# Performance work log

Measured on AMD Instinct MI355X. Metric: run time of the kernel, lower is better.

The kernel has to match this reference:

```python
import jax, jax.numpy as jnp
import numpy as np

LEAK = 0.01  # torch LeakyReLU default negative_slope
HALF_LOG_2PI = 0.5 * float(np.log(2.0 * np.pi))


def setup_inputs() -> dict:
    key = jax.random.key(0)
    ks = jax.random.split(key, 5)
    N, D = 8192, 512
    H = 2 * D
    x = jax.random.normal(ks[0], (N, D), dtype=jnp.float32)
    # small init so exp(logvar/2) stays well-behaved (mimics trained-net scale)
    W1 = jax.random.normal(ks[1], (H, H), dtype=jnp.float32) * 0.02
    b1 = jnp.zeros((H,), dtype=jnp.float32)
    W2 = jax.random.normal(ks[2], (H, H), dtype=jnp.float32) * 0.02
    b2 = jnp.zeros((H,), dtype=jnp.float32)
    eps = jax.random.normal(ks[3], (N, D), dtype=jnp.float32)
    return {"x": x, "W1": W1, "b1": b1, "W2": W2, "b2": b2, "eps": eps, "n": 4}


def reference(x, W1, b1, W2, b2, eps, n):
    N, D = x.shape
    # pairwise squared distances via the expansion identity (avoids [N,N,D] diff)
    sq = jnp.sum(x * x, axis=1)                       # [N]
    d = sq[:, None] + sq[None, :] - 2.0 * (x @ x.T)   # [N, N]
    # argsort(d)[:, :n] == indices of the n smallest distances per row
    _, subsets = jax.lax.top_k(-d, n)                 # [N, n]
    z = x[subsets]                                    # [N, n, D] gather
    mu_pool = jnp.mean(z, axis=1)                     # [N, D]
    mx_pool = jnp.max(z, axis=1)                      # [N, D]
    h = jnp.concatenate((mu_pool, mx_pool), axis=1)   # [N, 2D]
    # decoder: Linear -> LeakyReLU -> Linear (torch Linear: h @ W.T + b)
    h = h @ W1.T + b1
    h = jnp.where(h >= 0, h, LEAK * h)
    h = h @ W2.T + b2
    mu = h[:, :D]
    sigma = jnp.exp(h[:, D:] * 0.5)
    x_out = x + mu + sigma * eps                      # rsample
    entropy = jnp.mean(0.5 + HALF_LOG_2PI + jnp.log(sigma))
    rows = jnp.repeat(jnp.arange(N), n)
    sub_idx = (rows, subsets.reshape(-1))
    return (x_out, entropy, sub_idx)
```

## Files before the change

kernel.cpp:

```cpp
#include <hip/hip_runtime.h>
#include <math.h>

#define N_ROWS 8192
#define DIM 512
#define HID 1024
#define NSPLIT 16
#define SPLITC 512
#define NCT 4

typedef _Float16 f16x8 __attribute__((ext_vector_type(8)));
typedef _Float16 f16x4 __attribute__((ext_vector_type(4)));
typedef float f32x4 __attribute__((ext_vector_type(4)));

__device__ __forceinline__ bool dj_less(float d1, int j1, float d2, int j2) {
  return (d1 < d2) || (d1 == d2 && j1 < j2);
}
__device__ __forceinline__ unsigned umin32(unsigned a, unsigned b) { return a < b ? a : b; }
__device__ __forceinline__ unsigned umax32(unsigned a, unsigned b) { return a > b ? a : b; }

__device__ __forceinline__ void gload_lds16(const void* g, void* s) {
  __builtin_amdgcn_global_load_lds((const __attribute__((address_space(1))) void*)g,
                                   (__attribute__((address_space(3))) void*)s, 16, 0, 0);
}

#define S_SWZ(r) ((((r) & 3) ^ (((r) >> 2) & 3)))

#define INS4(K, xin)                                   \
  {                                                    \
    unsigned xx = (xin), t;                            \
    t = umin32(K[0], xx); xx = umax32(K[0], xx); K[0] = t; \
    t = umin32(K[1], xx); xx = umax32(K[1], xx); K[1] = t; \
    t = umin32(K[2], xx); xx = umax32(K[2], xx); K[2] = t; \
    K[3] = umin32(K[3], xx);                           \
  }

__global__ __launch_bounds__(256) void convert_kernel(const float* __restrict__ x,
                                                      const float* __restrict__ W1,
                                                      const float* __restrict__ W2,
                                                      _Float16* __restrict__ xh,
                                                      _Float16* __restrict__ W1f,
                                                      _Float16* __restrict__ W2f,
                                                      float* __restrict__ sq) {
  int bid = blockIdx.x;
  int tid = threadIdx.x;
  if (bid < 4096) {
    int g = bid * 256 + tid;
    float4 v = reinterpret_cast<const float4*>(x)[g];
    f16x4 hv = {(_Float16)v.x, (_Float16)v.y, (_Float16)v.z, (_Float16)v.w};
    reinterpret_cast<f16x4*>(xh)[g] = hv;
    float s = v.x * v.x + v.y * v.y + v.z * v.z + v.w * v.w;
    for (int off = 32; off > 0; off >>= 1) s += __shfl_down(s, off);
    __shared__ float red[4];
    if ((tid & 63) == 0) red[tid >> 6] = s;
    __syncthreads();
    if (tid == 0) sq[bid * 2] = red[0] + red[1];
    if (tid == 128) sq[bid * 2 + 1] = red[2] + red[3];
  } else {
    const float* src = (bid < 5120) ? W1 : W2;
    _Float16* dst = (bid < 5120) ? W1f : W2f;
    int g = ((bid < 5120) ? (bid - 4096) : (bid - 5120)) * 256 + tid;
    float4 v = reinterpret_cast<const float4*>(src)[g];
    f16x4 h = {(_Float16)v.x, (_Float16)v.y, (_Float16)v.z, (_Float16)v.w};
    reinterpret_cast<f16x4*>(dst)[g] = h;
  }
}

__global__ __launch_bounds__(256, 4) void dist_cand_mfma(const _Float16* __restrict__ xh,
                                                         const float* __restrict__ sq,
                                                         unsigned int* __restrict__ cand) {
  __shared__ __align__(16) char smem[34816];
  unsigned* DkA = (unsigned*)(smem + 16384);
  unsigned* DkB = (unsigned*)(smem + 25600);
  const int tid = threadIdx.x;
  const int lane = tid & 63;
  const int w = tid >> 6;
  const int wm = w >> 1, wn = w & 1;
  const int row0 = blockIdx.x * 128;
  const int js = blockIdx.y;

  int a_off[4], b_off[4];
#pragma unroll
  for (int m = 0; m < 4; ++m) {
    int r = wm * 64 + m * 16 + (lane & 15);
    a_off[m] = r * 64 + (((lane >> 4) ^ S_SWZ(r)) * 16);
  }
#pragma unroll
  for (int n = 0; n < 4; ++n) {
    int r = wn * 64 + n * 16 + (lane & 15);
    b_off[n] = r * 64 + (((lane >> 4) ^ S_SWZ(r)) * 16);
  }

  int goff[2], wb[2];
#pragma unroll
  for (int h = 0; h < 2; ++h) {
    int i = h * 256 + tid;
    int r = i >> 2, cs = i & 3;
    int c = cs ^ S_SWZ(r);
    goff[h] = r * 512 + c * 8;
    wb[h] = h * 4096 + w * 1024;
  }

  const int sr = tid >> 2;
  const int sc = tid & 3;
  const int slot = wn * 16 + (lane & 15);

  unsigned keys[2][4];
#pragma unroll
  for (int p = 0; p < 2; ++p)
#pragma unroll
    for (int q = 0; q < 4; ++q) keys[p][q] = 0xFFFFFFFFu;

  const _Float16* arow = xh + (size_t)row0 * DIM;

  f32x4 acc[4][4];

  auto stage = [&](int b, const _Float16* br, int kt) {
#pragma unroll
    for (int h = 0; h < 2; ++h) {
      int go = goff[h] + kt * 32;
      gload_lds16(arow + go, smem + b * 16384 + wb[h]);
      gload_lds16(br + go, smem + b * 16384 + 8192 + wb[h]);
    }
  };
  auto compute = [&](int b) {
    f16x8 bf[4];
#pragma unroll
    for (int n = 0; n < 4; ++n) bf[n] = *(const f16x8*)(smem + b * 16384 + 8192 + b_off[n]);
#pragma unroll
    for (int m = 0; m < 4; ++m) {
      f16x8 af = *(const f16x8*)(smem + b * 16384 + a_off[m]);
#pragma unroll
      for (int n = 0; n < 4; ++n)
        acc[m][n] = __builtin_amdgcn_mfma_f32_16x16x32_f16(af, bf[n], acc[m][n], 0, 0, 0);
    }
  };

  stage(0, xh + (size_t)(js * SPLITC) * DIM, 0);
  __syncthreads();

#pragma unroll 1
  for (int ct = 0; ct < NCT; ++ct) {
    const int c0 = js * SPLITC + ct * 128;
    const _Float16* brow = xh + (size_t)c0 * DIM;
#pragma unroll
    for (int m = 0; m < 4; ++m)
#pragma unroll
      for (int n = 0; n < 4; ++n) acc[m][n] = (f32x4)0.0f;

#pragma unroll 1
    for (int k = 0; k < 8; ++k) {
      stage(1, brow, 2 * k + 1);
      compute(0);
      __syncthreads();
      if (k < 7) stage(0, brow, 2 * k + 2);
      compute(1);
      __syncthreads();
    }

    stage(0, xh + (size_t)(js * SPLITC + ((ct + 1) & (NCT - 1)) * 128) * DIM, 0);

    float sqjb[4];
#pragma unroll
    for (int n = 0; n < 4; ++n) sqjb[n] = sq[c0 + wn * 64 + n * 16 + (lane & 15)] + 1024.0f;

#pragma unroll
    for (int p = 0; p < 2; ++p) {
      if (wm == p) {
#pragma unroll
        for (int m = 0; m < 4; ++m)
#pragma unroll
          for (int j = 0; j < 4; ++j) {
            int rl = m * 16 + ((lane >> 4) << 2) + j;
            unsigned u[4];
#pragma unroll
            for (int n = 0; n < 4; ++n) {
              float v = fmaf(-2.0f, acc[m][n][j], sqjb[n]);
              u[n] = (__float_as_uint(v) & 0xFFFFE000u) |
                     (unsigned)(c0 + wn * 64 + n * 16 + (lane & 15));
            }
            unsigned lo01 = umin32(u[0], u[1]), hi01 = umax32(u[0], u[1]);
            unsigned lo23 = umin32(u[2], u[3]), hi23 = umax32(u[2], u[3]);
            DkA[rl * 36 + slot] = umin32(lo01, lo23);
            DkB[rl * 36 + slot] = umin32(umax32(lo01, lo23), umin32(hi01, hi23));
          }
      }
      __syncthreads();
      {
        const uint4* pa = (const uint4*)&DkA[sr * 36 + sc * 8];
        const uint4* pb = (const uint4*)&DkB[sr * 36 + sc * 8];
        uint4 a0 = pa[0], a1 = pa[1], b0 = pb[0], b1 = pb[1];
        INS4(keys[p], a0.x); INS4(keys[p], a0.y); INS4(keys[p], a0.z); INS4(keys[p], a0.w);
        INS4(keys[p], a1.x); INS4(keys[p], a1.y); INS4(keys[p], a1.z); INS4(keys[p], a1.w);
        INS4(keys[p], b0.x); INS4(keys[p], b0.y); INS4(keys[p], b0.z); INS4(keys[p], b0.w);
        INS4(keys[p], b1.x); INS4(keys[p], b1.y); INS4(keys[p], b1.z); INS4(keys[p], b1.w);
      }
      __syncthreads();
    }
  }

#pragma unroll
  for (int p = 0; p < 2; ++p) {
    int row = row0 + p * 64 + sr;
    uint4 o;
    o.x = keys[p][0]; o.y = keys[p][1]; o.z = keys[p][2]; o.w = keys[p][3];
    *reinterpret_cast<uint4*>(&cand[(size_t)row * 256 + js * 16 + sc * 4]) = o;
  }
}

__global__ __launch_bounds__(64) void rescore_pool_kernel(const float* __restrict__ x,
                                                          const float* __restrict__ sq,
                                                          const unsigned int* __restrict__ cand,
                                                          float* __restrict__ orows,
                                                          float* __restrict__ osubs,
                                                          _Float16* __restrict__ h0) {
  const int row = blockIdx.x;
  const int lane = threadIdx.x;
  uint4 q = *reinterpret_cast<const uint4*>(&cand[(size_t)row * 256 + lane * 4]);
  unsigned cur = q.x, c1 = q.y, c2 = q.z, c3 = q.w;
  unsigned myj = 0;
#pragma unroll 1
  for (int r = 0; r < 16; ++r) {
    unsigned mn = cur;
#pragma unroll
    for (int off = 32; off > 0; off >>= 1)
      mn = umin32(mn, (unsigned)__shfl_xor((int)mn, off));
    if (cur == mn) { cur = c1; c1 = c2; c2 = c3; c3 = 0xFFFFFFFFu; }
    if (lane == r) myj = mn & 0x1FFFu;
  }

  const float4* xi = reinterpret_cast<const float4*>(x + (size_t)row * DIM);
  float4 xa = xi[lane];
  float4 xb = xi[lane + 64];
  float sqi = sq[row];

  float dme = 0.0f;
  int jme = 0;
#pragma unroll 1
  for (int c = 0; c < 16; ++c) {
    int j = __shfl((int)myj, c);
    const float4* xj = reinterpret_cast<const float4*>(x + (size_t)j * DIM);
    float4 ya = xj[lane];
    float4 yb = xj[lane + 64];
    float dot = xa.x * ya.x + xa.y * ya.y + xa.z * ya.z + xa.w * ya.w +
                xb.x * yb.x + xb.y * yb.y + xb.z * yb.z + xb.w * yb.w;
#pragma unroll
    for (int off = 32; off > 0; off >>= 1) dot += __shfl_xor(dot, off);
    float d = sqi + sq[j] - 2.0f * dot;
    if (lane == c) { dme = d; jme = j; }
  }

  int rank2 = 0;
#pragma unroll
  for (int k = 0; k < 16; ++k) {
    float dk = __shfl(dme, k);
    int jk = __shfl(jme, k);
    rank2 += dj_less(dk, jk, dme, jme) ? 1 : 0;
  }
  __shared__ int s4[4];
  if (lane < 16 && rank2 < 4) {
    s4[rank2] = jme;
    orows[row * 4 + rank2] = (float)row;
    osubs[row * 4 + rank2] = (float)jme;
  }
  __syncthreads();

  int j0 = s4[0], j1 = s4[1], j2 = s4[2], j3 = s4[3];
  int c = lane * 8;
  float4 z0a = *reinterpret_cast<const float4*>(&x[(size_t)j0 * DIM + c]);
  float4 z0b = *reinterpret_cast<const float4*>(&x[(size_t)j0 * DIM + c + 4]);
  float4 z1a = *reinterpret_cast<const float4*>(&x[(size_t)j1 * DIM + c]);
  float4 z1b = *reinterpret_cast<const float4*>(&x[(size_t)j1 * DIM + c + 4]);
  float4 z2a = *reinterpret_cast<const float4*>(&x[(size_t)j2 * DIM + c]);
  float4 z2b = *reinterpret_cast<const float4*>(&x[(size_t)j2 * DIM + c + 4]);
  float4 z3a = *reinterpret_cast<const float4*>(&x[(size_t)j3 * DIM + c]);
  float4 z3b = *reinterpret_cast<const float4*>(&x[(size_t)j3 * DIM + c + 4]);
  f16x8 mu, mx;
  mu[0] = (_Float16)((z0a.x + z1a.x + z2a.x + z3a.x) * 0.25f);
  mu[1] = (_Float16)((z0a.y + z1a.y + z2a.y + z3a.y) * 0.25f);
  mu[2] = (_Float16)((z0a.z + z1a.z + z2a.z + z3a.z) * 0.25f);
  mu[3] = (_Float16)((z0a.w + z1a.w + z2a.w + z3a.w) * 0.25f);
  mu[4] = (_Float16)((z0b.x + z1b.x + z2b.x + z3b.x) * 0.25f);
  mu[5] = (_Float16)((z0b.y + z1b.y + z2b.y + z3b.y) * 0.25f);
  mu[6] = (_Float16)((z0b.z + z1b.z + z2b.z + z3b.z) * 0.25f);
  mu[7] = (_Float16)((z0b.w + z1b.w + z2b.w + z3b.w) * 0.25f);
  mx[0] = (_Float16)fmaxf(fmaxf(z0a.x, z1a.x), fmaxf(z2a.x, z3a.x));
  mx[1] = (_Float16)fmaxf(fmaxf(z0a.y, z1a.y), fmaxf(z2a.y, z3a.y));
  mx[2] = (_Float16)fmaxf(fmaxf(z0a.z, z1a.z), fmaxf(z2a.z, z3a.z));
  mx[3] = (_Float16)fmaxf(fmaxf(z0a.w, z1a.w), fmaxf(z2a.w, z3a.w));
  mx[4] = (_Float16)fmaxf(fmaxf(z0b.x, z1b.x), fmaxf(z2b.x, z3b.x));
  mx[5] = (_Float16)fmaxf(fmaxf(z0b.y, z1b.y), fmaxf(z2b.y, z3b.y));
  mx[6] = (_Float16)fmaxf(fmaxf(z0b.z, z1b.z), fmaxf(z2b.z, z3b.z));
  mx[7] = (_Float16)fmaxf(fmaxf(z0b.w, z1b.w), fmaxf(z2b.w, z3b.w));
  *reinterpret_cast<f16x8*>(&h0[(size_t)row * HID + c]) = mu;
  *reinterpret_cast<f16x8*>(&h0[(size_t)row * HID + DIM + c]) = mx;
}

__global__ __launch_bounds__(256, 2) void gemm_mfma_kernel(const _Float16* __restrict__ A,
                                                           const _Float16* __restrict__ W,
                                                           const float* __restrict__ bias,
                                                           _Float16* __restrict__ out16,
                                                           int act) {
  __shared__ __align__(16) char smem[32768];
  const int tid = threadIdx.x;
  const int lane = tid & 63;
  const int w = tid >> 6;
  const int wm = w >> 1, wn = w & 1;
  const int row0 = blockIdx.x * 128;
  const int col0 = blockIdx.y * 128;

  int a_off[4], b_off[4];
#pragma unroll
  for (int m = 0; m < 4; ++m) {
    int r = wm * 64 + m * 16 + (lane & 15);
    a_off[m] = r * 64 + (((lane >> 4) ^ S_SWZ(r)) * 16);
  }
#pragma unroll
  for (int n = 0; n < 4; ++n) {
    int r = wn * 64 + n * 16 + (lane & 15);
    b_off[n] = r * 64 + (((lane >> 4) ^ S_SWZ(r)) * 16);
  }

  int goff[2], wb[2];
#pragma unroll
  for (int h = 0; h < 2; ++h) {
    int i = h * 256 + tid;
    int r = i >> 2, cs = i & 3;
    int c = cs ^ S_SWZ(r);
    goff[h] = r * HID + c * 8;
    wb[h] = h * 4096 + w * 1024;
  }

  const _Float16* arow = A + (size_t)row0 * HID;
  const _Float16* brow = W + (size_t)col0 * HID;

  f32x4 acc[4][4];
#pragma unroll
  for (int m = 0; m < 4; ++m)
#pragma unroll
    for (int n = 0; n < 4; ++n) acc[m][n] = (f32x4)0.0f;

  auto stage = [&](int b, int kt) {
#pragma unroll
    for (int h = 0; h < 2; ++h) {
      int go = goff[h] + kt * 32;
      gload_lds16(arow + go, smem + b * 16384 + wb[h]);
      gload_lds16(brow + go, smem + b * 16384 + 8192 + wb[h]);
    }
  };
  auto compute = [&](int b) {
    f16x8 bf[4];
#pragma unroll
    for (int n = 0; n < 4; ++n) bf[n] = *(const f16x8*)(smem + b * 16384 + 8192 + b_off[n]);
#pragma unroll
    for (int m = 0; m < 4; ++m) {
      f16x8 af = *(const f16x8*)(smem + b * 16384 + a_off[m]);
#pragma unroll
      for (int n = 0; n < 4; ++n)
        acc[m][n] = __builtin_amdgcn_mfma_f32_16x16x32_f16(af, bf[n], acc[m][n], 0, 0, 0);
    }
  };

  stage(0, 0);
  __syncthreads();
#pragma unroll 1
  for (int k = 0; k < 16; ++k) {
    stage(1, 2 * k + 1);
    compute(0);
    __syncthreads();
    if (k < 15) stage(0, 2 * k + 2);
    compute(1);
    __syncthreads();
  }

  float bv[4];
#pragma unroll
  for (int n = 0; n < 4; ++n) bv[n] = bias[col0 + wn * 64 + n * 16 + (lane & 15)];

#pragma unroll
  for (int m = 0; m < 4; ++m)
#pragma unroll
    for (int n = 0; n < 4; ++n) {
      int cl = col0 + wn * 64 + n * 16 + (lane & 15);
#pragma unroll
      for (int j = 0; j < 4; ++j) {
        int rl = row0 + wm * 64 + m * 16 + ((lane >> 4) << 2) + j;
        float v = acc[m][n][j] + bv[n];
        if (act && v < 0.0f) v *= 0.01f;
        out16[(size_t)rl * HID + cl] = (_Float16)v;
      }
    }
}

__global__ __launch_bounds__(256) void outgen_kernel(const float* __restrict__ x,
                                                     const _Float16* __restrict__ h2,
                                                     const float* __restrict__ eps,
                                                     float* __restrict__ xout,
                                                     float* __restrict__ partials) {
  int tid = threadIdx.x;
  int gid = blockIdx.x * 256 + tid;
  size_t base = (size_t)gid * 4;
  int i = (int)(base >> 9);
  int c = (int)(base & 511);
  float4 xv = *reinterpret_cast<const float4*>(&x[base]);
  float4 ev = *reinterpret_cast<const float4*>(&eps[base]);
  f16x4 muh = *reinterpret_cast<const f16x4*>(&h2[(size_t)i * HID + c]);
  f16x4 hsh = *reinterpret_cast<const f16x4*>(&h2[(size_t)i * HID + DIM + c]);
  float hs0 = (float)hsh[0], hs1 = (float)hsh[1], hs2 = (float)hsh[2], hs3 = (float)hsh[3];
  float4 xo;
  xo.x = xv.x + (float)muh[0] + expf(0.5f * hs0) * ev.x;
  xo.y = xv.y + (float)muh[1] + expf(0.5f * hs1) * ev.y;
  xo.z = xv.z + (float)muh[2] + expf(0.5f * hs2) * ev.z;
  xo.w = xv.w + (float)muh[3] + expf(0.5f * hs3) * ev.w;
  *reinterpret_cast<float4*>(&xout[base]) = xo;
  float lsum = hs0 + hs1 + hs2 + hs3;
  for (int off = 32; off > 0; off >>= 1) lsum += __shfl_down(lsum, off);
  __shared__ float red[4];
  if ((tid & 63) == 0) red[tid >> 6] = lsum;
  __syncthreads();
  if (tid == 0) partials[blockIdx.x] = red[0] + red[1] + red[2] + red[3];
}

__global__ __launch_bounds__(256) void entfin_kernel(const float* __restrict__ partials,
                                                     float* __restrict__ ent) {
  int t = threadIdx.x;
  float s = 0.0f;
  for (int q = 0; q < 16; ++q) s += partials[t + 256 * q];
  for (int off = 32; off > 0; off >>= 1) s += __shfl_down(s, off);
  __shared__ float red[4];
  if ((t & 63) == 0) red[t >> 6] = s;
  __syncthreads();
  if (t == 0)
    ent[0] = 0.5f + 0.9189385332046727f +
             0.5f * (red[0] + red[1] + red[2] + red[3]) / (8192.0f * 512.0f);
}

extern "C" void kernel_launch(void* const* d_in, const int* in_sizes, int n_in,
                              void* d_out, int out_size, void* d_ws, size_t ws_size,
                              hipStream_t stream) {
  const float* x = (const float*)d_in[0];
  const float* W1 = (const float*)d_in[1];
  const float* b1 = (const float*)d_in[2];
  const float* W2 = (const float*)d_in[3];
  const float* b2 = (const float*)d_in[4];
  const float* eps = (const float*)d_in[5];

  float* out = (float*)d_out;
  float* ws = (float*)d_ws;

  float* sq = ws;
  float* partials = ws + 40960;
  unsigned int* cand = (unsigned int*)(ws + 65536);
  _Float16* h2f = (_Float16*)(ws + 65536);
  _Float16* xh = (_Float16*)(ws + 8454144);
  _Float16* h0f = (_Float16*)(ws + 8454144);
  _Float16* h1f = (_Float16*)(ws + 12648448);
  _Float16* W1f = (_Float16*)(ws + 16842752);
  _Float16* W2f = (_Float16*)(ws + 17367040);

  float* xout = out;
  float* ent = out + (size_t)N_ROWS * DIM;
  float* orows = ent + 1;
  float* osubs = orows + (size_t)N_ROWS * 4;

  convert_kernel<<<6144, 256, 0, stream>>>(x, W1, W2, xh, W1f, W2f, sq);
  dist_cand_mfma<<<dim3(64, NSPLIT), 256, 0, stream>>>(xh, sq, cand);
  rescore_pool_kernel<<<N_ROWS, 64, 0, stream>>>(x, sq, cand, orows, osubs, h0f);
  gemm_mfma_kernel<<<dim3(64, 8), 256, 0, stream>>>(h0f, W1f, b1, h1f, 1);
  gemm_mfma_kernel<<<dim3(64, 8), 256, 0, stream>>>(h1f, W2f, b2, h2f, 0);
  outgen_kernel<<<4096, 256, 0, stream>>>(x, h2f, eps, xout, partials);
  entfin_kernel<<<1, 256, 0, stream>>>(partials, ent);
}
```

Baseline: 186.9 us.

## Use 8 waves per GEMM block and pack 4 rows per rescore block

The decoder GEMM now runs 512 threads (8 waves in a 4x2 layout), so each wave owns a 32x64 output sub-tile instead of 64x64. Each thread also issues one global-to-LDS load per operand per stage instead of two. This halves the accumulator registers per wave and doubles the waves available to hide latency. The rescore/pool kernel handles four rows per 256-thread block, one per wave, to cut the number of tiny blocks and launch overhead. In exchange, each B fragment read from LDS is reused across fewer MFMAs, so LDS traffic per MFMA rises.

After: 189.8 us. Within noise of the previous version (+1.6%).

```diff
diff --git a/kernel.cpp b/kernel.cpp
--- a/kernel.cpp
+++ b/kernel.cpp
@@ -207,14 +207,15 @@
   }
 }
 
-__global__ __launch_bounds__(64) void rescore_pool_kernel(const float* __restrict__ x,
-                                                          const float* __restrict__ sq,
-                                                          const unsigned int* __restrict__ cand,
-                                                          float* __restrict__ orows,
-                                                          float* __restrict__ osubs,
-                                                          _Float16* __restrict__ h0) {
-  const int row = blockIdx.x;
-  const int lane = threadIdx.x;
+__global__ __launch_bounds__(256) void rescore_pool_kernel(const float* __restrict__ x,
+                                                           const float* __restrict__ sq,
+                                                           const unsigned int* __restrict__ cand,
+                                                           float* __restrict__ orows,
+                                                           float* __restrict__ osubs,
+                                                           _Float16* __restrict__ h0) {
+  const int lane = threadIdx.x & 63;
+  const int wid = threadIdx.x >> 6;
+  const int row = blockIdx.x * 4 + wid;
   uint4 q = *reinterpret_cast<const uint4*>(&cand[(size_t)row * 256 + lane * 4]);
   unsigned cur = q.x, c1 = q.y, c2 = q.z, c3 = q.w;
   unsigned myj = 0;
@@ -256,15 +257,15 @@
     int jk = __shfl(jme, k);
     rank2 += dj_less(dk, jk, dme, jme) ? 1 : 0;
   }
-  __shared__ int s4[4];
+  __shared__ int s4[4][4];
   if (lane < 16 && rank2 < 4) {
-    s4[rank2] = jme;
+    s4[wid][rank2] = jme;
     orows[row * 4 + rank2] = (float)row;
     osubs[row * 4 + rank2] = (float)jme;
   }
   __syncthreads();
 
-  int j0 = s4[0], j1 = s4[1], j2 = s4[2], j3 = s4[3];
+  int j0 = s4[wid][0], j1 = s4[wid][1], j2 = s4[wid][2], j3 = s4[wid][3];
   int c = lane * 8;
   float4 z0a = *reinterpret_cast<const float4*>(&x[(size_t)j0 * DIM + c]);
   float4 z0b = *reinterpret_cast<const float4*>(&x[(size_t)j0 * DIM + c + 4]);
@@ -295,7 +296,7 @@
   *reinterpret_cast<f16x8*>(&h0[(size_t)row * HID + DIM + c]) = mx;
 }
 
-__global__ __launch_bounds__(256, 2) void gemm_mfma_kernel(const _Float16* __restrict__ A,
+__global__ __launch_bounds__(512, 2) void gemm_mfma_kernel(const _Float16* __restrict__ A,
                                                            const _Float16* __restrict__ W,
                                                            const float* __restrict__ bias,
                                                            _Float16* __restrict__ out16,
@@ -304,14 +305,15 @@
   const int tid = threadIdx.x;
   const int lane = tid & 63;
   const int w = tid >> 6;
-  const int wm = w >> 1, wn = w & 1;
+  const int wm = w >> 1;
+  const int wn = w & 1;
   const int row0 = blockIdx.x * 128;
   const int col0 = blockIdx.y * 128;
 
-  int a_off[4], b_off[4];
-#pragma unroll
-  for (int m = 0; m < 4; ++m) {
-    int r = wm * 64 + m * 16 + (lane & 15);
+  int a_off[2], b_off[4];
+#pragma unroll
+  for (int m = 0; m < 2; ++m) {
+    int r = wm * 32 + m * 16 + (lane & 15);
     a_off[m] = r * 64 + (((lane >> 4) ^ S_SWZ(r)) * 16);
   }
 #pragma unroll
@@ -320,39 +322,31 @@
     b_off[n] = r * 64 + (((lane >> 4) ^ S_SWZ(r)) * 16);
   }
 
-  int goff[2], wb[2];
-#pragma unroll
-  for (int h = 0; h < 2; ++h) {
-    int i = h * 256 + tid;
-    int r = i >> 2, cs = i & 3;
-    int c = cs ^ S_SWZ(r);
-    goff[h] = r * HID + c * 8;
-    wb[h] = h * 4096 + w * 1024;
-  }
+  int sgr = tid >> 2, scs = tid & 3;
+  int sgc = scs ^ S_SWZ(sgr);
+  int goff = sgr * HID + sgc * 8;
+  int wb = w * 1024;
 
   const _Float16* arow = A + (size_t)row0 * HID;
   const _Float16* brow = W + (size_t)col0 * HID;
 
-  f32x4 acc[4][4];
-#pragma unroll
-  for (int m = 0; m < 4; ++m)
+  f32x4 acc[2][4];
+#pragma unroll
+  for (int m = 0; m < 2; ++m)
 #pragma unroll
     for (int n = 0; n < 4; ++n) acc[m][n] = (f32x4)0.0f;
 
   auto stage = [&](int b, int kt) {
-#pragma unroll
-    for (int h = 0; h < 2; ++h) {
-      int go = goff[h] + kt * 32;
-      gload_lds16(arow + go, smem + b * 16384 + wb[h]);
-      gload_lds16(brow + go, smem + b * 16384 + 8192 + wb[h]);
-    }
+    int go = goff + kt * 32;
+    gload_lds16(arow + go, smem + b * 16384 + wb);
+    gload_lds16(brow + go, smem + b * 16384 + 8192 + wb);
   };
   auto compute = [&](int b) {
     f16x8 bf[4];
 #pragma unroll
     for (int n = 0; n < 4; ++n) bf[n] = *(const f16x8*)(smem + b * 16384 + 8192 + b_off[n]);
 #pragma unroll
-    for (int m = 0; m < 4; ++m) {
+    for (int m = 0; m < 2; ++m) {
       f16x8 af = *(const f16x8*)(smem + b * 16384 + a_off[m]);
 #pragma unroll
       for (int n = 0; n < 4; ++n)
@@ -377,13 +371,13 @@
   for (int n = 0; n < 4; ++n) bv[n] = bias[col0 + wn * 64 + n * 16 + (lane & 15)];
 
 #pragma unroll
-  for (int m = 0; m < 4; ++m)
+  for (int m = 0; m < 2; ++m)
 #pragma unroll
     for (int n = 0; n < 4; ++n) {
       int cl = col0 + wn * 64 + n * 16 + (lane & 15);
 #pragma unroll
       for (int j = 0; j < 4; ++j) {
-        int rl = row0 + wm * 64 + m * 16 + ((lane >> 4) << 2) + j;
+        int rl = row0 + wm * 32 + m * 16 + ((lane >> 4) << 2) + j;
         float v = acc[m][n][j] + bv[n];
         if (act && v < 0.0f) v *= 0.01f;
         out16[(size_t)rl * HID + cl] = (_Float16)v;
@@ -464,9 +458,9 @@
 
   convert_kernel<<<6144, 256, 0, stream>>>(x, W1, W2, xh, W1f, W2f, sq);
   dist_cand_mfma<<<dim3(64, NSPLIT), 256, 0, stream>>>(xh, sq, cand);
-  rescore_pool_kernel<<<N_ROWS, 64, 0, stream>>>(x, sq, cand, orows, osubs, h0f);
-  gemm_mfma_kernel<<<dim3(64, 8), 256, 0, stream>>>(h0f, W1f, b1, h1f, 1);
-  gemm_mfma_kernel<<<dim3(64, 8), 256, 0, stream>>>(h1f, W2f, b2, h2f, 0);
+  rescore_pool_kernel<<<N_ROWS / 4, 256, 0, stream>>>(x, sq, cand, orows, osubs, h0f);
+  gemm_mfma_kernel<<<dim3(64, 8), 512, 0, stream>>>(h0f, W1f, b1, h1f, 1);
+  gemm_mfma_kernel<<<dim3(64, 8), 512, 0, stream>>>(h1f, W2f, b2, h2f, 0);
   outgen_kernel<<<4096, 256, 0, stream>>>(x, h2f, eps, xout, partials);
   entfin_kernel<<<1, 256, 0, stream>>>(partials, ent);
 }
```

## Exploit distance matrix symmetry: compute upper-triangle tiles and emit candidates both ways

Applied to the files above, without the earlier changes.

The distance candidate kernel now launches one block per upper-triangular 128x128 tile pair (2080 blocks) instead of sweeping all column tiles. Each tile yields per-row top-4 candidates for the I rows and, for off-diagonal tiles, column-wise top-4 candidates for the J rows, which nearly halves the MFMA work of the x·xᵀ product. The cost is an extra transposed reduction through LDS, more scattered candidate writes, and a while-loop to decode the tile index. The rescore kernel is also repacked to four rows per 256-thread block.

Measured after the change: 209.5 us. 1.12x slower.

```diff
diff --git a/kernel.cpp b/kernel.cpp
--- a/kernel.cpp
+++ b/kernel.cpp
@@ -4,9 +4,6 @@
 #define N_ROWS 8192
 #define DIM 512
 #define HID 1024
-#define NSPLIT 16
-#define SPLITC 512
-#define NCT 4
 
 typedef _Float16 f16x8 __attribute__((ext_vector_type(8)));
 typedef _Float16 f16x4 __attribute__((ext_vector_type(4)));
@@ -65,28 +62,38 @@
   }
 }
 
-__global__ __launch_bounds__(256, 4) void dist_cand_mfma(const _Float16* __restrict__ xh,
-                                                         const float* __restrict__ sq,
-                                                         unsigned int* __restrict__ cand) {
+__global__ __launch_bounds__(256, 4) void dist_sym_mfma(const _Float16* __restrict__ xh,
+                                                        const float* __restrict__ sq,
+                                                        unsigned int* __restrict__ cand) {
   __shared__ __align__(16) char smem[34816];
   unsigned* DkA = (unsigned*)(smem + 16384);
   unsigned* DkB = (unsigned*)(smem + 25600);
+  unsigned* Pm = (unsigned*)(smem);
+  unsigned* Tk = (unsigned*)(smem + 16384);
   const int tid = threadIdx.x;
   const int lane = tid & 63;
   const int w = tid >> 6;
   const int wm = w >> 1, wn = w & 1;
-  const int row0 = blockIdx.x * 128;
-  const int js = blockIdx.y;
+  const int lo = lane & 15, hi = lane >> 4;
+
+  int It, Jt;
+  {
+    int rem = blockIdx.x;
+    int i = 0, c = 64;
+    while (rem >= c) { rem -= c; ++i; c = 64 - i; }
+    It = i;
+    Jt = i + rem;
+  }
 
   int a_off[4], b_off[4];
 #pragma unroll
   for (int m = 0; m < 4; ++m) {
-    int r = wm * 64 + m * 16 + (lane & 15);
+    int r = wm * 64 + m * 16 + lo;
     a_off[m] = r * 64 + (((lane >> 4) ^ S_SWZ(r)) * 16);
   }
 #pragma unroll
   for (int n = 0; n < 4; ++n) {
-    int r = wn * 64 + n * 16 + (lane & 15);
+    int r = wn * 64 + n * 16 + lo;
     b_off[n] = r * 64 + (((lane >> 4) ^ S_SWZ(r)) * 16);
   }
 
@@ -102,24 +109,23 @@
 
   const int sr = tid >> 2;
   const int sc = tid & 3;
-  const int slot = wn * 16 + (lane & 15);
-
-  unsigned keys[2][4];
-#pragma unroll
-  for (int p = 0; p < 2; ++p)
-#pragma unroll
-    for (int q = 0; q < 4; ++q) keys[p][q] = 0xFFFFFFFFu;
-
-  const _Float16* arow = xh + (size_t)row0 * DIM;
+  const int slot = wn * 16 + lo;
+
+  const _Float16* arow = xh + (size_t)(It * 128) * DIM;
+  const _Float16* brow = xh + (size_t)(Jt * 128) * DIM;
 
   f32x4 acc[4][4];
-
-  auto stage = [&](int b, const _Float16* br, int kt) {
+#pragma unroll
+  for (int m = 0; m < 4; ++m)
+#pragma unroll
+    for (int n = 0; n < 4; ++n) acc[m][n] = (f32x4)0.0f;
+
+  auto stage = [&](int b, int kt) {
 #pragma unroll
     for (int h = 0; h < 2; ++h) {
       int go = goff[h] + kt * 32;
       gload_lds16(arow + go, smem + b * 16384 + wb[h]);
-      gload_lds16(br + go, smem + b * 16384 + 8192 + wb[h]);
+      gload_lds16(brow + go, smem + b * 16384 + 8192 + wb[h]);
     }
   };
   auto compute = [&](int b) {
@@ -135,86 +141,119 @@
     }
   };
 
-  stage(0, xh + (size_t)(js * SPLITC) * DIM, 0);
+  stage(0, 0);
   __syncthreads();
-
 #pragma unroll 1
-  for (int ct = 0; ct < NCT; ++ct) {
-    const int c0 = js * SPLITC + ct * 128;
-    const _Float16* brow = xh + (size_t)c0 * DIM;
-#pragma unroll
-    for (int m = 0; m < 4; ++m)
-#pragma unroll
-      for (int n = 0; n < 4; ++n) acc[m][n] = (f32x4)0.0f;
-
-#pragma unroll 1
-    for (int k = 0; k < 8; ++k) {
-      stage(1, brow, 2 * k + 1);
-      compute(0);
-      __syncthreads();
-      if (k < 7) stage(0, brow, 2 * k + 2);
-      compute(1);
-      __syncthreads();
-    }
-
-    stage(0, xh + (size_t)(js * SPLITC + ((ct + 1) & (NCT - 1)) * 128) * DIM, 0);
-
-    float sqjb[4];
-#pragma unroll
-    for (int n = 0; n < 4; ++n) sqjb[n] = sq[c0 + wn * 64 + n * 16 + (lane & 15)] + 1024.0f;
-
-#pragma unroll
-    for (int p = 0; p < 2; ++p) {
-      if (wm == p) {
-#pragma unroll
-        for (int m = 0; m < 4; ++m)
-#pragma unroll
-          for (int j = 0; j < 4; ++j) {
-            int rl = m * 16 + ((lane >> 4) << 2) + j;
-            unsigned u[4];
-#pragma unroll
-            for (int n = 0; n < 4; ++n) {
-              float v = fmaf(-2.0f, acc[m][n][j], sqjb[n]);
-              u[n] = (__float_as_uint(v) & 0xFFFFE000u) |
-                     (unsigned)(c0 + wn * 64 + n * 16 + (lane & 15));
-            }
-            unsigned lo01 = umin32(u[0], u[1]), hi01 = umax32(u[0], u[1]);
-            unsigned lo23 = umin32(u[2], u[3]), hi23 = umax32(u[2], u[3]);
-            DkA[rl * 36 + slot] = umin32(lo01, lo23);
-            DkB[rl * 36 + slot] = umin32(umax32(lo01, lo23), umin32(hi01, hi23));
+  for (int k = 0; k < 8; ++k) {
+    stage(1, 2 * k + 1);
+    compute(0);
+    __syncthreads();
+    if (k < 7) stage(0, 2 * k + 2);
+    compute(1);
+    __syncthreads();
+  }
+
+  float sqjb[4];
+#pragma unroll
+  for (int n = 0; n < 4; ++n) sqjb[n] = sq[Jt * 128 + wn * 64 + n * 16 + lo] + 1024.0f;
+  float sqr[4][4];
+#pragma unroll
+  for (int m = 0; m < 4; ++m)
+#pragma unroll
+    for (int j = 0; j < 4; ++j)
+      sqr[m][j] = sq[It * 128 + wm * 64 + m * 16 + hi * 4 + j] + 1024.0f;
+
+#pragma unroll
+  for (int p = 0; p < 2; ++p) {
+    if (wm == p) {
+#pragma unroll
+      for (int m = 0; m < 4; ++m)
+#pragma unroll
+        for (int j = 0; j < 4; ++j) {
+          int rl = m * 16 + hi * 4 + j;
+          unsigned u[4];
+#pragma unroll
+          for (int n = 0; n < 4; ++n) {
+            float v = fmaf(-2.0f, acc[m][n][j], sqjb[n]);
+            u[n] = (__float_as_uint(v) & 0xFFFFE000u) |
+                   (unsigned)(Jt * 128 + wn * 64 + n * 16 + lo);
           }
-      }
-      __syncthreads();
-      {
-        const uint4* pa = (const uint4*)&DkA[sr * 36 + sc * 8];
-        const uint4* pb = (const uint4*)&DkB[sr * 36 + sc * 8];
-        uint4 a0 = pa[0], a1 = pa[1], b0 = pb[0], b1 = pb[1];
-        INS4(keys[p], a0.x); INS4(keys[p], a0.y); INS4(keys[p], a0.z); INS4(keys[p], a0.w);
-        INS4(keys[p], a1.x); INS4(keys[p], a1.y); INS4(keys[p], a1.z); INS4(keys[p], a1.w);
-        INS4(keys[p], b0.x); INS4(keys[p], b0.y); INS4(keys[p], b0.z); INS4(keys[p], b0.w);
-        INS4(keys[p], b1.x); INS4(keys[p], b1.y); INS4(keys[p], b1.z); INS4(keys[p], b1.w);
-      }
-      __syncthreads();
-    }
-  }
-
-#pragma unroll
-  for (int p = 0; p < 2; ++p) {
-    int row = row0 + p * 64 + sr;
-    uint4 o;
-    o.x = keys[p][0]; o.y = keys[p][1]; o.z = keys[p][2]; o.w = keys[p][3];
-    *reinterpret_cast<uint4*>(&cand[(size_t)row * 256 + js * 16 + sc * 4]) = o;
-  }
-}
-
-__global__ __launch_bounds__(64) void rescore_pool_kernel(const float* __restrict__ x,
-                                                          const float* __restrict__ sq,
-                                                          const unsigned int* __restrict__ cand,
-                                                          float* __restrict__ orows,
-                                                          float* __restrict__ osubs,
-                                                          _Float16* __restrict__ h0) {
-  const int row = blockIdx.x;
-  const int lane = threadIdx.x;
+          unsigned lo01 = umin32(u[0], u[1]), hi01 = umax32(u[0], u[1]);
+          unsigned lo23 = umin32(u[2], u[3]), hi23 = umax32(u[2], u[3]);
+          DkA[rl * 36 + slot] = umin32(lo01, lo23);
+          DkB[rl * 36 + slot] = umin32(umax32(lo01, lo23), umin32(hi01, hi23));
+        }
+    }
+    __syncthreads();
+    {
+      unsigned keysI[4] = {0xFFFFFFFFu, 0xFFFFFFFFu, 0xFFFFFFFFu, 0xFFFFFFFFu};
+      const uint4* pa = (const uint4*)&DkA[sr * 36 + sc * 8];
+      const uint4* pb = (const uint4*)&DkB[sr * 36 + sc * 8];
+      uint4 a0 = pa[0], a1 = pa[1], b0 = pb[0], b1 = pb[1];
+      INS4(keysI, a0.x); INS4(keysI, a0.y); INS4(keysI, a0.z); INS4(keysI, a0.w);
+      INS4(keysI, a1.x); INS4(keysI, a1.y); INS4(keysI, a1.z); INS4(keysI, a1.w);
+      INS4(keysI, b0.x); INS4(keysI, b0.y); INS4(keysI, b0.z); INS4(keysI, b0.w);
+      INS4(keysI, b1.x); INS4(keysI, b1.y); INS4(keysI, b1.z); INS4(keysI, b1.w);
+#pragma unroll
+      for (int q = 0; q < 4; ++q) Pm[(p * 64 + sr) * 17 + sc * 4 + q] = keysI[q];
+    }
+    __syncthreads();
+  }
+
+  {
+    int r = tid >> 1, half = tid & 1;
+    unsigned kk[16];
+#pragma unroll
+    for (int e = 0; e < 16; ++e) kk[e] = Pm[r * 17 + e];
+#pragma unroll
+    for (int i = 0; i < 8; ++i) {
+      unsigned ki = kk[half * 8 + i];
+      int rank = 0;
+#pragma unroll
+      for (int e = 0; e < 16; ++e) rank += (kk[e] < ki) ? 1 : 0;
+      if (rank < 4) cand[(size_t)(It * 128 + r) * 256 + Jt * 4 + rank] = ki;
+    }
+  }
+
+  if (It != Jt) {
+    __syncthreads();
+#pragma unroll
+    for (int n = 0; n < 4; ++n) {
+      unsigned K4[4] = {0xFFFFFFFFu, 0xFFFFFFFFu, 0xFFFFFFFFu, 0xFFFFFFFFu};
+#pragma unroll
+      for (int m = 0; m < 4; ++m)
+#pragma unroll
+        for (int j = 0; j < 4; ++j) {
+          float v = fmaf(-2.0f, acc[m][n][j], sqr[m][j]);
+          unsigned key = (__float_as_uint(v) & 0xFFFFE000u) |
+                         (unsigned)(It * 128 + wm * 64 + m * 16 + hi * 4 + j);
+          INS4(K4, key);
+        }
+      int coll = wn * 64 + n * 16 + lo;
+#pragma unroll
+      for (int q = 0; q < 4; ++q) Tk[coll * 33 + (wm * 4 + hi) * 4 + q] = K4[q];
+    }
+    __syncthreads();
+    if (tid < 128) {
+      unsigned K4[4] = {0xFFFFFFFFu, 0xFFFFFFFFu, 0xFFFFFFFFu, 0xFFFFFFFFu};
+#pragma unroll
+      for (int e = 0; e < 32; ++e) INS4(K4, Tk[tid * 33 + e]);
+#pragma unroll
+      for (int q = 0; q < 4; ++q)
+        cand[(size_t)(Jt * 128 + tid) * 256 + It * 4 + q] = K4[q];
+    }
+  }
+}
+
+__global__ __launch_bounds__(256) void rescore_pool_kernel(const float* __restrict__ x,
+                                                           const float* __restrict__ sq,
+                                                           const unsigned int* __restrict__ cand,
+                                                           float* __restrict__ orows,
+                                                           float* __restrict__ osubs,
+                                                           _Float16* __restrict__ h0) {
+  const int lane = threadIdx.x & 63;
+  const int wid = threadIdx.x >> 6;
+  const int row = blockIdx.x * 4 + wid;
   uint4 q = *reinterpret_cast<const uint4*>(&cand[(size_t)row * 256 + lane * 4]);
   unsigned cur = q.x, c1 = q.y, c2 = q.z, c3 = q.w;
   unsigned myj = 0;
@@ -256,15 +295,15 @@
     int jk = __shfl(jme, k);
     rank2 += dj_less(dk, jk, dme, jme) ? 1 : 0;
   }
-  __shared__ int s4[4];
+  __shared__ int s4[4][4];
   if (lane < 16 && rank2 < 4) {
-    s4[rank2] = jme;
+    s4[wid][rank2] = jme;
     orows[row * 4 + rank2] = (float)row;
     osubs[row * 4 + rank2] = (float)jme;
   }
   __syncthreads();
 
-  int j0 = s4[0], j1 = s4[1], j2 = s4[2], j3 = s4[3];
+  int j0 = s4[wid][0], j1 = s4[wid][1], j2 = s4[wid][2], j3 = s4[wid][3];
   int c = lane * 8;
   float4 z0a = *reinterpret_cast<const float4*>(&x[(size_t)j0 * DIM + c]);
   float4 z0b = *reinterpret_cast<const float4*>(&x[(size_t)j0 * DIM + c + 4]);
@@ -463,8 +502,8 @@
   float* osubs = orows + (size_t)N_ROWS * 4;
 
   convert_kernel<<<6144, 256, 0, stream>>>(x, W1, W2, xh, W1f, W2f, sq);
-  dist_cand_mfma<<<dim3(64, NSPLIT), 256, 0, stream>>>(xh, sq, cand);
-  rescore_pool_kernel<<<N_ROWS, 64, 0, stream>>>(x, sq, cand, orows, osubs, h0f);
+  dist_sym_mfma<<<2080, 256, 0, stream>>>(xh, sq, cand);
+  rescore_pool_kernel<<<N_ROWS / 4, 256, 0, stream>>>(x, sq, cand, orows, osubs, h0f);
   gemm_mfma_kernel<<<dim3(64, 8), 256, 0, stream>>>(h0f, W1f, b1, h1f, 1);
   gemm_mfma_kernel<<<dim3(64, 8), 256, 0, stream>>>(h1f, W2f, b2, h2f, 0);
   outgen_kernel<<<4096, 256, 0, stream>>>(x, h2f, eps, xout, partials);
```
